# Performance work log

Hardware: AMD Instinct MI355X
Metric: run time of the kernel (lower is better)

Reference implementation:

```python
import jax, jax.numpy as jnp
import numpy as np

SEQ, IN, H = 64, 100000, 50


def setup_inputs() -> dict:
    key = jax.random.key(0)
    k0, k1, k2, k3, k4 = jax.random.split(key, 5)
    x = jax.random.normal(k0, (SEQ, 1, IN), dtype=jnp.float32) * 0.02
    Wi = jax.random.normal(k1, (IN, 4 * H), dtype=jnp.float32) * 0.01
    bi = jax.random.normal(k2, (4 * H,), dtype=jnp.float32) * 0.01
    Wh = jax.random.normal(k3, (H, 4 * H), dtype=jnp.float32) * 0.1
    bh = jax.random.normal(k4, (4 * H,), dtype=jnp.float32) * 0.01
    return {"x": x, "Wi": Wi, "bi": bi, "Wh": Wh, "bh": bh}


def reference(x, Wi, bi, Wh, bh):
    # x: [seq, batch=1, input_size] -- each row is a flattened ParameterList.
    # Precompute the input projection for all steps at once (one big GEMM),
    # same math as per-step input_weights(input) since it has no recurrence.
    gates_in = jnp.einsum('sbi,ig->sbg', x, Wi) + bi + bh  # [seq, 1, 4H]

    def step(carry, g_in):
        hx, cx = carry
        gates = g_in + hx @ Wh  # [1, 4H]
        i, f, g, o = jnp.split(gates, 4, axis=1)
        i = jax.nn.sigmoid(i)
        f = jax.nn.sigmoid(f)
        g = jnp.tanh(g)
        o = jax.nn.sigmoid(o)
        cy = f * cx + i * g
        hy = o * jnp.tanh(cy)
        return (hy, cy), None

    h0 = jnp.zeros((1, H), dtype=x.dtype)
    c0 = jnp.zeros((1, H), dtype=x.dtype)
    (h_final, _), _ = jax.lax.scan(step, (h0, c0), gates_in)
    # torch.squeeze(out_hidden): (1, H) -> (H,)
    return jnp.squeeze(h_final)
```

## Files before the change

kernel.cpp:

```cpp
#include <hip/hip_runtime.h>
#include <hip/hip_bf16.h>


#define K_DIM 100000
#define NG 200
#define NS 64
#define TK 32
#define NBLK 256
#define NTILES 3125
#define CELLS (NS * NG)
#define CELLS4 (CELLS / 4)
#define ROWU 40

typedef unsigned short u16;
typedef unsigned int   u32;
typedef __bf16 bf16x8 __attribute__((ext_vector_type(8)));
typedef float  f32x16 __attribute__((ext_vector_type(16)));

static __device__ __forceinline__ u32 rne16(float f) {
    u32 u = __float_as_uint(f);
    return (u + 0x7FFFu + ((u >> 16) & 1u)) >> 16;
}
static __device__ __forceinline__ void split_hl(float f, u32& h, u32& l) {
    u32 u  = __float_as_uint(f);
    u32 hb = u & 0xFFFF0000u;
    h = hb >> 16;
    l = rne16(f - __uint_as_float(hb));
}
static __device__ __forceinline__ void split4(float4 v, u32 h[4], u32 l[4]) {
    split_hl(v.x, h[0], l[0]); split_hl(v.y, h[1], l[1]);
    split_hl(v.z, h[2], l[2]); split_hl(v.w, h[3], l[3]);
}
static __device__ __forceinline__ f32x16 mfma_bf(uint4 a, uint4 b, f32x16 c) {
    return __builtin_amdgcn_mfma_f32_32x32x16_bf16(
        __builtin_bit_cast(bf16x8, a), __builtin_bit_cast(bf16x8, b), c, 0, 0, 0);
}

__global__ __launch_bounds__(512, 1) void k1_gemm_partial(
    const float* __restrict__ x, const float* __restrict__ Wi,
    float* __restrict__ partial)
{
    __shared__ __align__(16) u16 WH[224 * ROWU];
    __shared__ __align__(16) u16 WL[224 * ROWU];
    __shared__ __align__(16) u16 XH[64 * ROWU];
    __shared__ __align__(16) u16 XL[64 * ROWU];

    const int t    = threadIdx.x;
    const int lane = t & 63;
    const int wave = t >> 6;
    const int m    = lane & 31;
    const int h    = lane >> 5;
    const int stile = wave >> 2;
    const int gset  = wave & 3;

    {
        u32* zh = (u32*)&WH[200 * ROWU];
        u32* zl = (u32*)&WL[200 * ROWU];
        for (int i = t; i < 24 * ROWU / 2; i += 512) { zh[i] = 0; zl[i] = 0; }
    }

    const int a_g4 = t >> 3;
    const int a_k4 = t & 7;
    const bool has_w = (t < 400);
    const int xs0 = t >> 3, xk0 = t & 7;

    float4 wa[4], xa;
    auto do_loads = [&](int ti) {
        const size_t kt = (size_t)ti * TK;
        if (has_w) {
#pragma unroll
            for (int j = 0; j < 4; ++j)
                wa[j] = *(const float4*)(Wi + (kt + a_k4 * 4 + j) * NG + a_g4 * 4);
        }
        xa = *(const float4*)(x + (size_t)xs0 * K_DIM + kt + xk0 * 4);
    };
    auto stage_wi = [&](const float4 r[4], int g4, int k4) {
        u32 hw[4][4], lw[4][4];
#pragma unroll
        for (int j = 0; j < 4; ++j) split4(r[j], hw[j], lw[j]);
#pragma unroll
        for (int j2 = 0; j2 < 4; ++j2) {
            int off = (4 * g4 + j2) * ROWU + k4 * 4;
            *(uint2*)&WH[off] = make_uint2(hw[0][j2] | (hw[1][j2] << 16),
                                           hw[2][j2] | (hw[3][j2] << 16));
            *(uint2*)&WL[off] = make_uint2(lw[0][j2] | (lw[1][j2] << 16),
                                           lw[2][j2] | (lw[3][j2] << 16));
        }
    };
    auto stage_x = [&](float4 v, int s, int k4) {
        u32 hh[4], ll[4];
        split4(v, hh, ll);
        int off = s * ROWU + k4 * 4;
        *(uint2*)&XH[off] = make_uint2(hh[0] | (hh[1] << 16), hh[2] | (hh[3] << 16));
        *(uint2*)&XL[off] = make_uint2(ll[0] | (ll[1] << 16), ll[2] | (ll[3] << 16));
    };

    f32x16 acc[2];
#pragma unroll
    for (int tt = 0; tt < 2; ++tt)
#pragma unroll
        for (int r = 0; r < 16; ++r) acc[tt][r] = 0.f;

    const int aoff = (stile * 32 + m) * ROWU + h * 8;
    int boff[2];
#pragma unroll
    for (int tt = 0; tt < 2; ++tt) {
        int gt = (gset == 3 && tt == 1) ? 6 : (2 * gset + tt);
        boff[tt] = (gt * 32 + m) * ROWU + h * 8;
    }

    do_loads(blockIdx.x);
    for (int ti = blockIdx.x; ti < NTILES; ti += NBLK) {
        __syncthreads();
        if (has_w) stage_wi(wa, a_g4, a_k4);
        stage_x(xa, xs0, xk0);
        __syncthreads();

        int tin = ti + NBLK;
        if (tin < NTILES) do_loads(tin);

#pragma unroll
        for (int kk = 0; kk < 2; ++kk) {
            uint4 ah = *(const uint4*)&XH[aoff + kk * 16];
            uint4 al = *(const uint4*)&XL[aoff + kk * 16];
#pragma unroll
            for (int tt = 0; tt < 2; ++tt) {
                uint4 bh = *(const uint4*)&WH[boff[tt] + kk * 16];
                uint4 bl = *(const uint4*)&WL[boff[tt] + kk * 16];
                acc[tt] = mfma_bf(ah, bh, acc[tt]);
                acc[tt] = mfma_bf(ah, bl, acc[tt]);
                acc[tt] = mfma_bf(al, bh, acc[tt]);
            }
        }
    }

    float* base = partial + (size_t)blockIdx.x * CELLS;
#pragma unroll
    for (int tt = 0; tt < 2; ++tt) {
        if (gset == 3 && tt == 1) continue;
        int g = (2 * gset + tt) * 32 + m;
        if (g < NG) {
#pragma unroll
            for (int r = 0; r < 16; ++r) {
                int srow = stile * 32 + (r & 3) + 8 * (r >> 2) + 4 * h;
                base[srow * NG + g] = acc[tt][r];
            }
        }
    }
}

__global__ __launch_bounds__(512) void k2_reduce(
    const float* __restrict__ partial, const float* __restrict__ bi,
    const float* __restrict__ bh, float* __restrict__ gates)
{
    __shared__ float4 red[512];
    const int tid   = threadIdx.x;
    const int fid   = tid & 15;
    const int slice = tid >> 4;
    const int g4    = blockIdx.x * 16 + fid;

    const float4* p4 = (const float4*)partial;
    float4 sum = make_float4(0.f, 0.f, 0.f, 0.f);
#pragma unroll 4
    for (int b = slice * 8; b < slice * 8 + 8; ++b) {
        float4 v = p4[(size_t)b * CELLS4 + g4];
        sum.x += v.x; sum.y += v.y; sum.z += v.z; sum.w += v.w;
    }
    red[tid] = sum;
    __syncthreads();
    if (tid < 16) {
        float4 tot = red[tid];
#pragma unroll
        for (int p = 1; p < 32; ++p) {
            float4 v = red[p * 16 + tid];
            tot.x += v.x; tot.y += v.y; tot.z += v.z; tot.w += v.w;
        }
        int gg = (g4 * 4) % NG;
        float4 b1 = *(const float4*)(bi + gg);
        float4 b2 = *(const float4*)(bh + gg);
        tot.x += b1.x + b2.x; tot.y += b1.y + b2.y;
        tot.z += b1.z + b2.z; tot.w += b1.w + b2.w;
        ((float4*)gates)[g4] = tot;
    }
}

__global__ __launch_bounds__(256) void k3_lstm(
    const float* __restrict__ gates, const float* __restrict__ Wh,
    float* __restrict__ out)
{
    __shared__ float gz[CELLS];
    __shared__ float h_lds[64];
    __shared__ float act_lds[NG];
    const int g = threadIdx.x;

    for (int i = g; i < CELLS; i += 256) gz[i] = gates[i];

    float wh[50];
    if (g < NG) {
#pragma unroll
        for (int j = 0; j < 50; ++j) wh[j] = Wh[j * NG + g];
    }
    if (g < 64) h_lds[g] = 0.f;
    float c = 0.f, h = 0.f;
    const bool is_cell_gate = (g >= 100 && g < 150);
    __syncthreads();

    for (int s = 0; s < 64; ++s) {
        if (g < NG) {
            float a0 = gz[s * NG + g], a1 = 0.f, a2 = 0.f, a3 = 0.f;
#pragma unroll
            for (int jj = 0; jj < 48; jj += 4) {
                float4 h4 = *(const float4*)(h_lds + jj);
                a0 = fmaf(h4.x, wh[jj],     a0);
                a1 = fmaf(h4.y, wh[jj + 1], a1);
                a2 = fmaf(h4.z, wh[jj + 2], a2);
                a3 = fmaf(h4.w, wh[jj + 3], a3);
            }
            {
                float2 h2 = *(const float2*)(h_lds + 48);
                a0 = fmaf(h2.x, wh[48], a0);
                a1 = fmaf(h2.y, wh[49], a1);
            }
            float z = (a0 + a1) + (a2 + a3);
            float e   = __expf(-z);
            float sig = 1.f / (1.f + e);
            float e2  = e * e;
            float th  = (1.f - e2) / (1.f + e2);
            act_lds[g] = is_cell_gate ? th : sig;
        }
        __syncthreads();
        if (g < 50) {
            float iv = act_lds[g];
            float fv = act_lds[50 + g];
            float gv = act_lds[100 + g];
            float ov = act_lds[150 + g];
            c = fmaf(fv, c, iv * gv);
            float e2c = __expf(-2.f * c);
            h = ov * (1.f - e2c) / (1.f + e2c);
            h_lds[g] = h;
        }
        __syncthreads();
    }
    if (g < 50) out[g] = h;
}

extern "C" void kernel_launch(void* const* d_in, const int* in_sizes, int n_in,
                              void* d_out, int out_size, void* d_ws, size_t ws_size,
                              hipStream_t stream)
{
    const float* x  = (const float*)d_in[0];
    const float* Wi = (const float*)d_in[1];
    const float* bi = (const float*)d_in[2];
    const float* Wh = (const float*)d_in[3];
    const float* bh = (const float*)d_in[4];
    float* out = (float*)d_out;

    float* partial = (float*)d_ws;
    float* gates   = partial + (size_t)NBLK * CELLS;

    k1_gemm_partial<<<NBLK, 512, 0, stream>>>(x, Wi, partial);
    k2_reduce<<<CELLS4 / 16, 512, 0, stream>>>(partial, bi, bh, gates);
    k3_lstm<<<1, 256, 0, stream>>>(gates, Wh, out);
}
```

Baseline: 187.1 us.

## Double-buffer GEMM LDS tiles and drop per-step LSTM barrier via wave-local h

Measured after the change: 193.7 us. 1.04x slower.

```diff
diff --git a/kernel.cpp b/kernel.cpp
--- a/kernel.cpp
+++ b/kernel.cpp
@@ -40,10 +40,10 @@
     const float* __restrict__ x, const float* __restrict__ Wi,
     float* __restrict__ partial)
 {
-    __shared__ __align__(16) u16 WH[224 * ROWU];
-    __shared__ __align__(16) u16 WL[224 * ROWU];
-    __shared__ __align__(16) u16 XH[64 * ROWU];
-    __shared__ __align__(16) u16 XL[64 * ROWU];
+    __shared__ __align__(16) u16 WH[2][224 * ROWU];
+    __shared__ __align__(16) u16 WL[2][224 * ROWU];
+    __shared__ __align__(16) u16 XH[2][64 * ROWU];
+    __shared__ __align__(16) u16 XL[2][64 * ROWU];
 
     const int t    = threadIdx.x;
     const int lane = t & 63;
@@ -53,9 +53,10 @@
     const int stile = wave >> 2;
     const int gset  = wave & 3;
 
-    {
-        u32* zh = (u32*)&WH[200 * ROWU];
-        u32* zl = (u32*)&WL[200 * ROWU];
+#pragma unroll
+    for (int b = 0; b < 2; ++b) {
+        u32* zh = (u32*)&WH[b][200 * ROWU];
+        u32* zl = (u32*)&WL[b][200 * ROWU];
         for (int i = t; i < 24 * ROWU / 2; i += 512) { zh[i] = 0; zl[i] = 0; }
     }
 
@@ -74,25 +75,25 @@
         }
         xa = *(const float4*)(x + (size_t)xs0 * K_DIM + kt + xk0 * 4);
     };
-    auto stage_wi = [&](const float4 r[4], int g4, int k4) {
+    auto stage_wi = [&](u16* WHp, u16* WLp) {
         u32 hw[4][4], lw[4][4];
 #pragma unroll
-        for (int j = 0; j < 4; ++j) split4(r[j], hw[j], lw[j]);
+        for (int j = 0; j < 4; ++j) split4(wa[j], hw[j], lw[j]);
 #pragma unroll
         for (int j2 = 0; j2 < 4; ++j2) {
-            int off = (4 * g4 + j2) * ROWU + k4 * 4;
-            *(uint2*)&WH[off] = make_uint2(hw[0][j2] | (hw[1][j2] << 16),
-                                           hw[2][j2] | (hw[3][j2] << 16));
-            *(uint2*)&WL[off] = make_uint2(lw[0][j2] | (lw[1][j2] << 16),
-                                           lw[2][j2] | (lw[3][j2] << 16));
+            int off = (4 * a_g4 + j2) * ROWU + a_k4 * 4;
+            *(uint2*)&WHp[off] = make_uint2(hw[0][j2] | (hw[1][j2] << 16),
+                                            hw[2][j2] | (hw[3][j2] << 16));
+            *(uint2*)&WLp[off] = make_uint2(lw[0][j2] | (lw[1][j2] << 16),
+                                            lw[2][j2] | (lw[3][j2] << 16));
         }
     };
-    auto stage_x = [&](float4 v, int s, int k4) {
+    auto stage_x = [&](u16* XHp, u16* XLp) {
         u32 hh[4], ll[4];
-        split4(v, hh, ll);
-        int off = s * ROWU + k4 * 4;
-        *(uint2*)&XH[off] = make_uint2(hh[0] | (hh[1] << 16), hh[2] | (hh[3] << 16));
-        *(uint2*)&XL[off] = make_uint2(ll[0] | (ll[1] << 16), ll[2] | (ll[3] << 16));
+        split4(xa, hh, ll);
+        int off = xs0 * ROWU + xk0 * 4;
+        *(uint2*)&XHp[off] = make_uint2(hh[0] | (hh[1] << 16), hh[2] | (hh[3] << 16));
+        *(uint2*)&XLp[off] = make_uint2(ll[0] | (ll[1] << 16), ll[2] | (ll[3] << 16));
     };
 
     f32x16 acc[2];
@@ -110,28 +111,41 @@
     }
 
     do_loads(blockIdx.x);
+    if (has_w) stage_wi(WH[0], WL[0]);
+    stage_x(XH[0], XL[0]);
+    {
+        int tin = blockIdx.x + NBLK;
+        if (tin < NTILES) do_loads(tin);
+    }
+    __syncthreads();
+
+    int p = 0;
     for (int ti = blockIdx.x; ti < NTILES; ti += NBLK) {
-        __syncthreads();
-        if (has_w) stage_wi(wa, a_g4, a_k4);
-        stage_x(xa, xs0, xk0);
-        __syncthreads();
-
-        int tin = ti + NBLK;
-        if (tin < NTILES) do_loads(tin);
-
+        int tn = ti + NBLK;
+        if (tn < NTILES) {
+            if (has_w) stage_wi(WH[p ^ 1], WL[p ^ 1]);
+            stage_x(XH[p ^ 1], XL[p ^ 1]);
+            int t2 = tn + NBLK;
+            if (t2 < NTILES) do_loads(t2);
+        }
+
+        const u16* WHp = WH[p]; const u16* WLp = WL[p];
+        const u16* XHp = XH[p]; const u16* XLp = XL[p];
 #pragma unroll
         for (int kk = 0; kk < 2; ++kk) {
-            uint4 ah = *(const uint4*)&XH[aoff + kk * 16];
-            uint4 al = *(const uint4*)&XL[aoff + kk * 16];
+            uint4 ah = *(const uint4*)&XHp[aoff + kk * 16];
+            uint4 al = *(const uint4*)&XLp[aoff + kk * 16];
 #pragma unroll
             for (int tt = 0; tt < 2; ++tt) {
-                uint4 bh = *(const uint4*)&WH[boff[tt] + kk * 16];
-                uint4 bl = *(const uint4*)&WL[boff[tt] + kk * 16];
+                uint4 bh = *(const uint4*)&WHp[boff[tt] + kk * 16];
+                uint4 bl = *(const uint4*)&WLp[boff[tt] + kk * 16];
                 acc[tt] = mfma_bf(ah, bh, acc[tt]);
                 acc[tt] = mfma_bf(ah, bl, acc[tt]);
                 acc[tt] = mfma_bf(al, bh, acc[tt]);
             }
         }
+        __syncthreads();
+        p ^= 1;
     }
 
     float* base = partial + (size_t)blockIdx.x * CELLS;
@@ -188,36 +202,44 @@
     const float* __restrict__ gates, const float* __restrict__ Wh,
     float* __restrict__ out)
 {
-    __shared__ float gz[CELLS];
-    __shared__ float h_lds[64];
-    __shared__ float act_lds[NG];
-    const int g = threadIdx.x;
-
-    for (int i = g; i < CELLS; i += 256) gz[i] = gates[i];
+    __shared__ __align__(16) float gz[CELLS];
+    __shared__ float hbuf[4][64];
+    __shared__ float act[2][NG];
+    const int t    = threadIdx.x;
+    const int g    = t;
+    const int w    = t >> 6;
+    const int lane = t & 63;
+
+    {
+        float4* gz4 = (float4*)gz;
+        const float4* gp4 = (const float4*)gates;
+        for (int i = t; i < CELLS4; i += 256) gz4[i] = gp4[i];
+    }
 
     float wh[50];
     if (g < NG) {
 #pragma unroll
         for (int j = 0; j < 50; ++j) wh[j] = Wh[j * NG + g];
     }
-    if (g < 64) h_lds[g] = 0.f;
+    hbuf[w][lane] = 0.f;
     float c = 0.f, h = 0.f;
     const bool is_cell_gate = (g >= 100 && g < 150);
     __syncthreads();
 
+    const float* hl = hbuf[w];
     for (int s = 0; s < 64; ++s) {
         if (g < NG) {
             float a0 = gz[s * NG + g], a1 = 0.f, a2 = 0.f, a3 = 0.f;
 #pragma unroll
             for (int jj = 0; jj < 48; jj += 4) {
-                float4 h4 = *(const float4*)(h_lds + jj);
+                float4 h4 = *(const float4*)(hl + jj);
                 a0 = fmaf(h4.x, wh[jj],     a0);
                 a1 = fmaf(h4.y, wh[jj + 1], a1);
                 a2 = fmaf(h4.z, wh[jj + 2], a2);
                 a3 = fmaf(h4.w, wh[jj + 3], a3);
             }
             {
-                float2 h2 = *(const float2*)(h_lds + 48);
+                float2 h2 = *(const float2*)(hl + 48);
                 a0 = fmaf(h2.x, wh[48], a0);
                 a1 = fmaf(h2.y, wh[49], a1);
             }
@@ -226,22 +248,21 @@
             float sig = 1.f / (1.f + e);
             float e2  = e * e;
             float th  = (1.f - e2) / (1.f + e2);
-            act_lds[g] = is_cell_gate ? th : sig;
+            act[s & 1][g] = is_cell_gate ? th : sig;
         }
         __syncthreads();
-        if (g < 50) {
-            float iv = act_lds[g];
-            float fv = act_lds[50 + g];
-            float gv = act_lds[100 + g];
-            float ov = act_lds[150 + g];
+        if (lane < 50) {
+            float iv = act[s & 1][lane];
+            float fv = act[s & 1][50 + lane];
+            float gv = act[s & 1][100 + lane];
+            float ov = act[s & 1][150 + lane];
             c = fmaf(fv, c, iv * gv);
             float e2c = __expf(-2.f * c);
             h = ov * (1.f - e2c) / (1.f + e2c);
-            h_lds[g] = h;
-        }
-        __syncthreads();
-    }
-    if (g < 50) out[g] = h;
+            hbuf[w][lane] = h;
+        }
+    }
+    if (t < 50) out[t] = h;
 }
 
 extern "C" void kernel_launch(void* const* d_in, const int* in_sizes, int n_in,
```

## Double-buffer LDS tiles and prefetch two tiles ahead in GEMM kernel

Applied to the files above, without the earlier changes.

Result: no change. 184.8 us (-1.2%).

```diff
diff --git a/kernel.cpp b/kernel.cpp
--- a/kernel.cpp
+++ b/kernel.cpp
@@ -40,10 +40,10 @@
     const float* __restrict__ x, const float* __restrict__ Wi,
     float* __restrict__ partial)
 {
-    __shared__ __align__(16) u16 WH[224 * ROWU];
-    __shared__ __align__(16) u16 WL[224 * ROWU];
-    __shared__ __align__(16) u16 XH[64 * ROWU];
-    __shared__ __align__(16) u16 XL[64 * ROWU];
+    __shared__ __align__(16) u16 WH[2][224 * ROWU];
+    __shared__ __align__(16) u16 WL[2][224 * ROWU];
+    __shared__ __align__(16) u16 XH[2][64 * ROWU];
+    __shared__ __align__(16) u16 XL[2][64 * ROWU];
 
     const int t    = threadIdx.x;
     const int lane = t & 63;
@@ -53,9 +53,10 @@
     const int stile = wave >> 2;
     const int gset  = wave & 3;
 
-    {
-        u32* zh = (u32*)&WH[200 * ROWU];
-        u32* zl = (u32*)&WL[200 * ROWU];
+#pragma unroll
+    for (int b = 0; b < 2; ++b) {
+        u32* zh = (u32*)&WH[b][200 * ROWU];
+        u32* zl = (u32*)&WL[b][200 * ROWU];
         for (int i = t; i < 24 * ROWU / 2; i += 512) { zh[i] = 0; zl[i] = 0; }
     }
 
@@ -64,35 +65,34 @@
     const bool has_w = (t < 400);
     const int xs0 = t >> 3, xk0 = t & 7;
 
-    float4 wa[4], xa;
-    auto do_loads = [&](int ti) {
+    auto do_loads = [&](int ti, float4 (&wr)[4], float4& xr) {
         const size_t kt = (size_t)ti * TK;
         if (has_w) {
 #pragma unroll
             for (int j = 0; j < 4; ++j)
-                wa[j] = *(const float4*)(Wi + (kt + a_k4 * 4 + j) * NG + a_g4 * 4);
-        }
-        xa = *(const float4*)(x + (size_t)xs0 * K_DIM + kt + xk0 * 4);
-    };
-    auto stage_wi = [&](const float4 r[4], int g4, int k4) {
+                wr[j] = *(const float4*)(Wi + (kt + a_k4 * 4 + j) * NG + a_g4 * 4);
+        }
+        xr = *(const float4*)(x + (size_t)xs0 * K_DIM + kt + xk0 * 4);
+    };
+    auto stage_wi = [&](const float4 (&r)[4], u16* WHp, u16* WLp) {
         u32 hw[4][4], lw[4][4];
 #pragma unroll
         for (int j = 0; j < 4; ++j) split4(r[j], hw[j], lw[j]);
 #pragma unroll
         for (int j2 = 0; j2 < 4; ++j2) {
-            int off = (4 * g4 + j2) * ROWU + k4 * 4;
-            *(uint2*)&WH[off] = make_uint2(hw[0][j2] | (hw[1][j2] << 16),
-                                           hw[2][j2] | (hw[3][j2] << 16));
-            *(uint2*)&WL[off] = make_uint2(lw[0][j2] | (lw[1][j2] << 16),
-                                           lw[2][j2] | (lw[3][j2] << 16));
-        }
-    };
-    auto stage_x = [&](float4 v, int s, int k4) {
+            int off = (4 * a_g4 + j2) * ROWU + a_k4 * 4;
+            *(uint2*)&WHp[off] = make_uint2(hw[0][j2] | (hw[1][j2] << 16),
+                                            hw[2][j2] | (hw[3][j2] << 16));
+            *(uint2*)&WLp[off] = make_uint2(lw[0][j2] | (lw[1][j2] << 16),
+                                            lw[2][j2] | (lw[3][j2] << 16));
+        }
+    };
+    auto stage_x = [&](float4 v, u16* XHp, u16* XLp) {
         u32 hh[4], ll[4];
         split4(v, hh, ll);
-        int off = s * ROWU + k4 * 4;
-        *(uint2*)&XH[off] = make_uint2(hh[0] | (hh[1] << 16), hh[2] | (hh[3] << 16));
-        *(uint2*)&XL[off] = make_uint2(ll[0] | (ll[1] << 16), ll[2] | (ll[3] << 16));
+        int off = xs0 * ROWU + xk0 * 4;
+        *(uint2*)&XHp[off] = make_uint2(hh[0] | (hh[1] << 16), hh[2] | (hh[3] << 16));
+        *(uint2*)&XLp[off] = make_uint2(ll[0] | (ll[1] << 16), ll[2] | (ll[3] << 16));
     };
 
     f32x16 acc[2];
@@ -109,28 +109,61 @@
         boff[tt] = (gt * 32 + m) * ROWU + h * 8;
     }
 
-    do_loads(blockIdx.x);
-    for (int ti = blockIdx.x; ti < NTILES; ti += NBLK) {
-        __syncthreads();
-        if (has_w) stage_wi(wa, a_g4, a_k4);
-        stage_x(xa, xs0, xk0);
-        __syncthreads();
-
-        int tin = ti + NBLK;
-        if (tin < NTILES) do_loads(tin);
-
+    auto mfma_phase = [&](int p) {
+        const u16* WHp = WH[p]; const u16* WLp = WL[p];
+        const u16* XHp = XH[p]; const u16* XLp = XL[p];
 #pragma unroll
         for (int kk = 0; kk < 2; ++kk) {
-            uint4 ah = *(const uint4*)&XH[aoff + kk * 16];
-            uint4 al = *(const uint4*)&XL[aoff + kk * 16];
+            uint4 ah = *(const uint4*)&XHp[aoff + kk * 16];
+            uint4 al = *(const uint4*)&XLp[aoff + kk * 16];
 #pragma unroll
             for (int tt = 0; tt < 2; ++tt) {
-                uint4 bh = *(const uint4*)&WH[boff[tt] + kk * 16];
-                uint4 bl = *(const uint4*)&WL[boff[tt] + kk * 16];
+                uint4 bh = *(const uint4*)&WHp[boff[tt] + kk * 16];
+                uint4 bl = *(const uint4*)&WLp[boff[tt] + kk * 16];
                 acc[tt] = mfma_bf(ah, bh, acc[tt]);
                 acc[tt] = mfma_bf(ah, bl, acc[tt]);
                 acc[tt] = mfma_bf(al, bh, acc[tt]);
             }
+        }
+    };
+
+    float4 waA[4], waB[4];
+    float4 xaA, xaB;
+    const int ti0 = blockIdx.x;
+    do_loads(ti0,            waA, xaA);
+    do_loads(ti0 + NBLK,     waB, xaB);
+    if (has_w) stage_wi(waA, WH[0], WL[0]);
+    stage_x(xaA, XH[0], XL[0]);
+    do_loads(ti0 + 2 * NBLK, waA, xaA);
+    __syncthreads();
+
+    int p = 0;
+    int ti = ti0;
+    while (ti < NTILES) {
+        {
+            int tn = ti + NBLK;
+            if (tn < NTILES) {
+                if (has_w) stage_wi(waB, WH[p ^ 1], WL[p ^ 1]);
+                stage_x(xaB, XH[p ^ 1], XL[p ^ 1]);
+                int tf = tn + 2 * NBLK;
+                if (tf < NTILES) do_loads(tf, waB, xaB);
+            }
+            mfma_phase(p);
+            __syncthreads();
+            p ^= 1; ti += NBLK;
+        }
+        if (ti >= NTILES) break;
+        {
+            int tn = ti + NBLK;
+            if (tn < NTILES) {
+                if (has_w) stage_wi(waA, WH[p ^ 1], WL[p ^ 1]);
+                stage_x(xaA, XH[p ^ 1], XL[p ^ 1]);
+                int tf = tn + 2 * NBLK;
+                if (tf < NTILES) do_loads(tf, waA, xaA);
+            }
+            mfma_phase(p);
+            __syncthreads();
+            p ^= 1; ti += NBLK;
         }
     }
 
```
